# Optimization experiments

Measured on AMD Instinct MI355X. Metric: run time of the kernel, lower is better.

The kernel has to match this reference:

```python
import jax, jax.numpy as jnp
import numpy as np

N_WIRES = 13
N_LAYERS = 3
N_OUT = 10
T = 1.0
BATCH = 512
DIM = 2 ** N_WIRES
TWO_PI = 2.0 * np.pi

# Z eigenvalue table: Z_TAB[s, i] = +1 if bit of wire i in basis state s is 0 else -1.
# PennyLane convention: wire 0 is the most-significant bit of the statevector index.
_bits = (np.arange(DIM)[:, None] >> (N_WIRES - 1 - np.arange(N_WIRES))) & 1
Z_TAB = jnp.asarray(1.0 - 2.0 * _bits, dtype=jnp.float32)        # (DIM, n)
ZZ_TAB = Z_TAB * jnp.roll(Z_TAB, -1, axis=1)                     # z_i * z_{(i+1)%n}


def rot_matrix(phi, theta, omega):
    # qml.Rot = RZ(omega) @ RY(theta) @ RZ(phi)
    c = jnp.cos(theta / 2)
    s = jnp.sin(theta / 2)
    ep = jnp.exp(-0.5j * (phi + omega).astype(jnp.complex64))
    em = jnp.exp(-0.5j * (phi - omega).astype(jnp.complex64))
    row0 = jnp.stack([ep * c, -jnp.conj(em) * s])
    row1 = jnp.stack([em * s, jnp.conj(ep) * c])
    return jnp.stack([row0, row1])  # (2, 2) complex64


def apply_1q(state, U, w):
    # state: (B, 2, 2, ..., 2); apply 2x2 gate U on wire w (axis w+1)
    st = jnp.moveaxis(state, w + 1, 1)
    st = jnp.einsum('ab,xb...->xa...', U, st)
    return jnp.moveaxis(st, 1, w + 1)


def apply_cnot(state, c, t):
    # flip target axis where control bit == 1
    st = jnp.moveaxis(state, (c + 1, t + 1), (1, 2))
    st = jnp.concatenate([st[:, :1], st[:, 1:, ::-1]], axis=1)
    return jnp.moveaxis(st, (1, 2), (c + 1, t + 1))


def _forward(inputs, weights, embed_weights):
    B = inputs.shape[0]
    # Hadamard on every wire from |0...0> -> uniform superposition
    psi = jnp.full((B, DIM), DIM ** -0.5, dtype=jnp.complex64)
    for l in range(N_LAYERS):
        # --- Hamiltonian encoding: diagonal phase exp(-i t (sum (w x + b) Z_i + sum g Z_i Z_{i+1}))
        omega = embed_weights[l, :, 0]
        bias = embed_weights[l, :, 1]
        gamma = embed_weights[l, :, 2]
        coeff = inputs * omega + bias                              # (B, n)
        ang = T * (coeff @ Z_TAB.T + gamma @ ZZ_TAB.T)             # (B, DIM)
        psi = psi * jnp.exp((-1j) * ang.astype(jnp.complex64))
        # --- StronglyEntanglingLayers, single layer (range 1)
        st = psi.reshape((B,) + (2,) * N_WIRES)
        for i in range(N_WIRES):
            U = rot_matrix(weights[l, i, 0], weights[l, i, 1], weights[l, i, 2])
            st = apply_1q(st, U, i)
        for i in range(N_WIRES):
            st = apply_cnot(st, i, (i + 1) % N_WIRES)
        psi = st.reshape(B, DIM)
    probs = psi.real ** 2 + psi.imag ** 2                          # (B, DIM)
    return probs @ Z_TAB[:, :N_OUT]                                # <Z_i>, (B, N_OUT)


def setup_inputs() -> dict:
    key = jax.random.key(0)
    k1, k2, k3 = jax.random.split(key, 3)
    inputs = jax.random.normal(k1, (BATCH, N_WIRES), dtype=jnp.float32)
    weights = jax.random.uniform(k2, (N_LAYERS, N_WIRES, 3), dtype=jnp.float32) * TWO_PI
    embed_weights = jax.random.uniform(k3, (N_LAYERS, N_WIRES, 3), dtype=jnp.float32) * TWO_PI
    return {"inputs": inputs, "weights": weights, "embed_weights": embed_weights}


def reference(inputs, weights, embed_weights):
    return _forward(inputs, weights, embed_weights)
```

## Files before the change

kernel.cpp:

```cpp
#include <hip/hip_runtime.h>
#include <math.h>

#define N_WIRES 13
#define DIM 8192
#define N_LAYERS 3
#define N_OUT 10
#define BATCH 512
#define NTHREADS 512

typedef float v2f __attribute__((ext_vector_type(2)));

#define CMUL_PK(d, u, a) do { \
    asm("v_pk_mul_f32 %0, %1, %2 op_sel:[0,0] op_sel_hi:[0,1]" \
        : "=v"(d) : "v"(u), "v"(a)); \
    asm("v_pk_fma_f32 %0, %1, %2, %0 op_sel:[1,1,0] op_sel_hi:[1,0,1] neg_lo:[0,1,0]" \
        : "+v"(d) : "v"(u), "v"(a)); \
} while (0)

#define CFMA_PK(d, u, a) do { \
    asm("v_pk_fma_f32 %0, %1, %2, %0 op_sel:[0,0,0] op_sel_hi:[0,1,1]" \
        : "+v"(d) : "v"(u), "v"(a)); \
    asm("v_pk_fma_f32 %0, %1, %2, %0 op_sel:[1,1,0] op_sel_hi:[1,0,1] neg_lo:[0,1,0]" \
        : "+v"(d) : "v"(u), "v"(a)); \
} while (0)

__device__ __forceinline__ void bfly(v2f& a0, v2f& a1,
                                     v2f u00, v2f u01, v2f u10, v2f u11) {
    v2f n0, n1;
    CMUL_PK(n0, u00, a0); CFMA_PK(n0, u01, a1);
    CMUL_PK(n1, u10, a0); CFMA_PK(n1, u11, a1);
    a0 = n0; a1 = n1;
}

#define REG_GATE(MASK, W) do { \
    const float4 uA = uu4[l][W][0]; \
    const float4 uB = uu4[l][W][1]; \
    const v2f u00 = {uA.x, uA.y}, u01 = {uA.z, uA.w}; \
    const v2f u10 = {uB.x, uB.y}, u11 = {uB.z, uB.w}; \
    _Pragma("unroll") \
    for (int k0 = 0; k0 < 16; ++k0) { \
        if (k0 & (MASK)) continue; \
        bfly(a[k0], a[k0 | (MASK)], u00, u01, u10, u11); \
    } \
} while (0)

#define SWZ1_GATE(W) do { \
    const float4 uA = uu4[l][W][0]; \
    const float4 uB = uu4[l][W][1]; \
    const bool hb = (tid & 1) != 0; \
    const v2f ua = hb ? (v2f){uB.z, uB.w} : (v2f){uA.x, uA.y}; \
    const v2f up = hb ? (v2f){uB.x, uB.y} : (v2f){uA.z, uA.w}; \
    _Pragma("unroll") \
    for (int k = 0; k < 16; ++k) { \
        v2f p; \
        p.x = __int_as_float(__builtin_amdgcn_ds_swizzle(__float_as_int(a[k].x), 0x041F)); \
        p.y = __int_as_float(__builtin_amdgcn_ds_swizzle(__float_as_int(a[k].y), 0x041F)); \
        v2f n; CMUL_PK(n, ua, a[k]); CFMA_PK(n, up, p); \
        a[k] = n; \
    } \
} while (0)

__global__ __launch_bounds__(NTHREADS, 2) void vqc_kernel(
    const float* __restrict__ inputs,
    const float* __restrict__ weights,
    const float* __restrict__ embed,
    float* __restrict__ out)
{
    __shared__ v2f  s2[DIM];
    __shared__ float4 uu4[N_LAYERS][N_WIRES][2];
    __shared__ float  co[N_LAYERS][N_WIRES];
    __shared__ float  ga[N_LAYERS][N_WIRES];
    __shared__ v2f  Ek[N_LAYERS][16];
    __shared__ v2f  Eh[N_LAYERS][8];
    __shared__ v2f  El[N_LAYERS][64];
    __shared__ v2f  G3[N_LAYERS], G12[N_LAYERS], G6[N_LAYERS];
    __shared__ float red[NTHREADS / 64][N_OUT];

    const int b   = blockIdx.x;
    const int tid = threadIdx.x;

    if (tid < N_LAYERS * N_WIRES) {
        const int l = tid / N_WIRES;
        const int w = tid - l * N_WIRES;
        const int base = (l * N_WIRES + w) * 3;
        const float om = embed[base + 0];
        const float bi = embed[base + 1];
        const float gm = embed[base + 2];
        co[l][w] = inputs[b * N_WIRES + w] * om + bi;
        ga[l][w] = gm;

        const float phi = weights[base + 0];
        const float th  = weights[base + 1];
        const float omg = weights[base + 2];
        float c, s, ca, sa, cb, sb;
        __sincosf(0.5f * th, &s, &c);
        __sincosf(0.5f * (phi + omg), &sa, &ca);
        __sincosf(0.5f * (phi - omg), &sb, &cb);
        uu4[l][w][0] = make_float4( ca * c, -sa * c, -cb * s, -sb * s);
        uu4[l][w][1] = make_float4( cb * s, -sb * s,  ca * c,  sa * c);

        if (w == 3 || w == 6 || w == 12) {
            float s2v, c2v; __sincosf(2.f * gm, &s2v, &c2v);
            if (w == 3)  G3[l]  = (v2f){c2v, s2v};
            if (w == 6)  G6[l]  = (v2f){c2v, s2v};
            if (w == 12) G12[l] = (v2f){c2v, s2v};
        }
    }
    __syncthreads();

    if (tid < N_LAYERS * 16) {
        const int l = tid >> 4, k = tid & 15;
        float S = 0.f;
        #pragma unroll
        for (int w = 0; w < N_WIRES; ++w) S += co[l][w] + ga[l][w];
        const int b3 = (k >> 3) & 1, b2 = (k >> 2) & 1, b1 = (k >> 1) & 1, b0 = k & 1;
        float v = S;
        if (b3) v -= 2.f * co[l][0];
        if (b2) v -= 2.f * co[l][1];
        if (b1) v -= 2.f * co[l][2];
        if (b0) v -= 2.f * co[l][3];
        if (b3 ^ b2) v -= 2.f * ga[l][0];
        if (b2 ^ b1) v -= 2.f * ga[l][1];
        if (b1 ^ b0) v -= 2.f * ga[l][2];
        float sv, cv; __sincosf(v, &sv, &cv);
        const float sc = (l == 0) ? 0.011048543456039806f : 1.f;
        Ek[l][k] = (v2f){sc * cv, -sc * sv};
    }
    if (tid >= 64 && tid < 64 + N_LAYERS * 8) {
        const int t = tid - 64, l = t >> 3, h = t & 7;
        const int b8 = (h >> 2) & 1, b7 = (h >> 1) & 1, b6 = h & 1;
        float T = 0.f;
        if (b8) T += co[l][4];
        if (b7) T += co[l][5];
        if (b6) T += co[l][6];
        if (b8 ^ b7) T += ga[l][4];
        if (b7 ^ b6) T += ga[l][5];
        float sv, cv; __sincosf(2.f * T, &sv, &cv);
        Eh[l][h] = (v2f){cv, sv};
    }
    if (tid >= 128 && tid < 128 + N_LAYERS * 64) {
        const int t = tid - 128, l = t >> 6, m = t & 63;
        const int b5 = (m >> 5) & 1, b4 = (m >> 4) & 1, b3 = (m >> 3) & 1;
        const int b2 = (m >> 2) & 1, b1 = (m >> 1) & 1, b0 = m & 1;
        float T = 0.f;
        if (b5) T += co[l][7];
        if (b4) T += co[l][8];
        if (b3) T += co[l][9];
        if (b2) T += co[l][10];
        if (b1) T += co[l][11];
        if (b0) T += co[l][12];
        if (b5 ^ b4) T += ga[l][7];
        if (b4 ^ b3) T += ga[l][8];
        if (b3 ^ b2) T += ga[l][9];
        if (b2 ^ b1) T += ga[l][10];
        if (b1 ^ b0) T += ga[l][11];
        float sv, cv; __sincosf(2.f * T, &sv, &cv);
        El[l][m] = (v2f){cv, sv};
    }
    __syncthreads();

    const int tidA   = tid ^ ((tid >> 5) & 0xE);
    const int baseB  = ((tid >> 5) << 9) | (tid & 31);
    const int xbaseC = ((tid >> 1) << 5) | (tid & 1);
    const int baseC  = xbaseC ^ ((tid >> 1) & 0xE);
    const bool t8 = ((tid >> 8) & 1) != 0;
    const bool t0 = (tid & 1) != 0;
    const bool cG6 = (((tid >> 6) ^ (tid >> 5)) & 1) != 0;
    const int hidx = (tid >> 6) & 7;
    const int lidx = tid & 63;

    v2f a[16];

    #pragma unroll 1
    for (int l = 0; l < N_LAYERS; ++l) {
        v2f ep; CMUL_PK(ep, Eh[l][hidx], El[l][lidx]);
        { v2f t6; CMUL_PK(t6, ep, G6[l]); ep = cG6 ? t6 : ep; }
        v2f eg3; CMUL_PK(eg3, ep, G3[l]);
        const v2f P0 = t8 ? eg3 : ep,  P1 = t8 ? ep : eg3;
        const v2f one = {1.f, 0.f};
        const v2f Q0 = t0 ? G12[l] : one, Q1 = t0 ? one : G12[l];
        v2f R00, R01, R10, R11;
        CMUL_PK(R00, P0, Q0);
        CMUL_PK(R01, P0, Q1);
        CMUL_PK(R10, P1, Q0);
        CMUL_PK(R11, P1, Q1);

        if (l == 0) {
            #pragma unroll
            for (int k = 0; k < 16; ++k) {
                const v2f Rk = (k & 1) ? ((k & 8) ? R11 : R10) : ((k & 8) ? R01 : R00);
                CMUL_PK(a[k], Rk, Ek[l][k]);
            }
        } else {
            #pragma unroll
            for (int k = 0; k < 16; ++k) {
                const v2f Rk = (k & 1) ? ((k & 8) ? R11 : R10) : ((k & 8) ? R01 : R00);
                v2f f; CMUL_PK(f, Rk, Ek[l][k]);
                const v2f v = s2[tidA | (k << 9)];
                CMUL_PK(a[k], v, f);
            }
        }

        REG_GATE(8, 0);
        REG_GATE(4, 1);
        REG_GATE(2, 2);
        REG_GATE(1, 3);

        #pragma unroll
        for (int k = 0; k < 16; ++k)
            s2[tidA | (k << 9)] = a[k];
        __syncthreads();

        #pragma unroll
        for (int k = 0; k < 16; ++k)
            a[k] = s2[baseB ^ ((k << 5) | (k & 0xE))];
        REG_GATE(8, 4);
        REG_GATE(4, 5);
        REG_GATE(2, 6);
        REG_GATE(1, 7);
        #pragma unroll
        for (int k = 0; k < 16; ++k)
            s2[baseB ^ ((k << 5) | (k & 0xE))] = a[k];
        __syncthreads();

        #pragma unroll
        for (int k = 0; k < 16; ++k)
            a[k] = s2[baseC ^ (k << 1)];
        if (l < N_LAYERS - 1) __syncthreads();

        REG_GATE(8, 8);
        REG_GATE(4, 9);
        REG_GATE(2, 10);
        REG_GATE(1, 11);
        SWZ1_GATE(12);

        if (l < N_LAYERS - 1) {
            #pragma unroll
            for (int k = 0; k < 16; ++k) {
                const int x = xbaseC | (k << 1);
                int t = x ^ (x >> 1); t ^= t >> 2; t ^= t >> 4; t ^= t >> 8;
                const int y = (t & 0x0FFF) | (((t ^ (x >> 12)) & 1) << 12);
                s2[y ^ ((y >> 5) & 0xE)] = a[k];
            }
            __syncthreads();
        }
    }

    float acc[N_OUT];
    #pragma unroll
    for (int o = 0; o < N_OUT; ++o) acc[o] = 0.f;

    #pragma unroll
    for (int k = 0; k < 16; ++k) {
        const int x = xbaseC | (k << 1);
        int t = x ^ (x >> 1); t ^= t >> 2; t ^= t >> 4; t ^= t >> 8;
        const int y = (t & 0x0FFF) | (((t ^ (x >> 12)) & 1) << 12);
        const float p = a[k].x * a[k].x + a[k].y * a[k].y;
        #pragma unroll
        for (int o = 0; o < N_OUT; ++o)
            acc[o] += ((y >> (12 - o)) & 1) ? -p : p;
    }

    #pragma unroll
    for (int off = 32; off >= 1; off >>= 1) {
        #pragma unroll
        for (int o = 0; o < N_OUT; ++o) acc[o] += __shfl_down(acc[o], off);
    }
    const int wave = tid >> 6;
    const int lane = tid & 63;
    if (lane == 0) {
        #pragma unroll
        for (int o = 0; o < N_OUT; ++o) red[wave][o] = acc[o];
    }
    __syncthreads();
    if (tid < N_OUT) {
        float s = 0.f;
        #pragma unroll
        for (int w = 0; w < NTHREADS / 64; ++w) s += red[w][tid];
        out[b * N_OUT + tid] = s;
    }
}

extern "C" void kernel_launch(void* const* d_in, const int* in_sizes, int n_in,
                              void* d_out, int out_size, void* d_ws, size_t ws_size,
                              hipStream_t stream) {
    const float* inputs  = (const float*)d_in[0];
    const float* weights = (const float*)d_in[1];
    const float* embed   = (const float*)d_in[2];
    float* out = (float*)d_out;
    vqc_kernel<<<BATCH, NTHREADS, 0, stream>>>(inputs, weights, embed, out);
}
```

Measured before the change: 52.60 us.

## Double threads per block, hold 8 amplitudes per thread with four gate phases

The block grows from 512 to 1024 threads, so each thread keeps 8 amplitudes in registers instead of 16. The 12 register-resident wire gates are regrouped from three phases of four wires into four phases of three, each with new swizzled shared-memory index maps. The diagonal phase tables are resplit to match (Ek over 3 wires, Eh over 4). This halves register pressure per thread and adds parallelism, at the cost of one extra shared-memory round trip and barrier per layer, and of larger blocks that need wider synchronisation.

Result: faster. 47.49 us (-9.7%).

```diff
diff --git a/kernel.cpp b/kernel.cpp
--- a/kernel.cpp
+++ b/kernel.cpp
@@ -6,7 +6,9 @@
 #define N_LAYERS 3
 #define N_OUT 10
 #define BATCH 512
-#define NTHREADS 512
+#define NTHREADS 1024
+#define NAMPS 8
+#define NWAVES (NTHREADS / 64)
 
 typedef float v2f __attribute__((ext_vector_type(2)));
 
@@ -38,7 +40,7 @@
     const v2f u00 = {uA.x, uA.y}, u01 = {uA.z, uA.w}; \
     const v2f u10 = {uB.x, uB.y}, u11 = {uB.z, uB.w}; \
     _Pragma("unroll") \
-    for (int k0 = 0; k0 < 16; ++k0) { \
+    for (int k0 = 0; k0 < NAMPS; ++k0) { \
         if (k0 & (MASK)) continue; \
         bfly(a[k0], a[k0 | (MASK)], u00, u01, u10, u11); \
     } \
@@ -51,7 +53,7 @@
     const v2f ua = hb ? (v2f){uB.z, uB.w} : (v2f){uA.x, uA.y}; \
     const v2f up = hb ? (v2f){uB.x, uB.y} : (v2f){uA.z, uA.w}; \
     _Pragma("unroll") \
-    for (int k = 0; k < 16; ++k) { \
+    for (int k = 0; k < NAMPS; ++k) { \
         v2f p; \
         p.x = __int_as_float(__builtin_amdgcn_ds_swizzle(__float_as_int(a[k].x), 0x041F)); \
         p.y = __int_as_float(__builtin_amdgcn_ds_swizzle(__float_as_int(a[k].y), 0x041F)); \
@@ -60,7 +62,7 @@
     } \
 } while (0)
 
-__global__ __launch_bounds__(NTHREADS, 2) void vqc_kernel(
+__global__ __launch_bounds__(NTHREADS, 8) void vqc_kernel(
     const float* __restrict__ inputs,
     const float* __restrict__ weights,
     const float* __restrict__ embed,
@@ -70,11 +72,11 @@
     __shared__ float4 uu4[N_LAYERS][N_WIRES][2];
     __shared__ float  co[N_LAYERS][N_WIRES];
     __shared__ float  ga[N_LAYERS][N_WIRES];
-    __shared__ v2f  Ek[N_LAYERS][16];
-    __shared__ v2f  Eh[N_LAYERS][8];
+    __shared__ v2f  Ek[N_LAYERS][8];
+    __shared__ v2f  Eh[N_LAYERS][16];
     __shared__ v2f  El[N_LAYERS][64];
-    __shared__ v2f  G3[N_LAYERS], G12[N_LAYERS], G6[N_LAYERS];
-    __shared__ float red[NTHREADS / 64][N_OUT];
+    __shared__ v2f  G2[N_LAYERS], G6b[N_LAYERS], G12[N_LAYERS];
+    __shared__ float red[NWAVES][N_OUT];
 
     const int b   = blockIdx.x;
     const int tid = threadIdx.x;
@@ -99,42 +101,42 @@
         uu4[l][w][0] = make_float4( ca * c, -sa * c, -cb * s, -sb * s);
         uu4[l][w][1] = make_float4( cb * s, -sb * s,  ca * c,  sa * c);
 
-        if (w == 3 || w == 6 || w == 12) {
+        if (w == 2 || w == 6 || w == 12) {
             float s2v, c2v; __sincosf(2.f * gm, &s2v, &c2v);
-            if (w == 3)  G3[l]  = (v2f){c2v, s2v};
-            if (w == 6)  G6[l]  = (v2f){c2v, s2v};
+            if (w == 2)  G2[l]  = (v2f){c2v, s2v};
+            if (w == 6)  G6b[l] = (v2f){c2v, s2v};
             if (w == 12) G12[l] = (v2f){c2v, s2v};
         }
     }
     __syncthreads();
 
-    if (tid < N_LAYERS * 16) {
-        const int l = tid >> 4, k = tid & 15;
+    if (tid < N_LAYERS * 8) {
+        const int l = tid >> 3, k = tid & 7;
         float S = 0.f;
         #pragma unroll
         for (int w = 0; w < N_WIRES; ++w) S += co[l][w] + ga[l][w];
-        const int b3 = (k >> 3) & 1, b2 = (k >> 2) & 1, b1 = (k >> 1) & 1, b0 = k & 1;
+        const int b2 = (k >> 2) & 1, b1 = (k >> 1) & 1, b0 = k & 1;
         float v = S;
-        if (b3) v -= 2.f * co[l][0];
-        if (b2) v -= 2.f * co[l][1];
-        if (b1) v -= 2.f * co[l][2];
-        if (b0) v -= 2.f * co[l][3];
-        if (b3 ^ b2) v -= 2.f * ga[l][0];
-        if (b2 ^ b1) v -= 2.f * ga[l][1];
-        if (b1 ^ b0) v -= 2.f * ga[l][2];
+        if (b2) v -= 2.f * co[l][0];
+        if (b1) v -= 2.f * co[l][1];
+        if (b0) v -= 2.f * co[l][2];
+        if (b2 ^ b1) v -= 2.f * ga[l][0];
+        if (b1 ^ b0) v -= 2.f * ga[l][1];
         float sv, cv; __sincosf(v, &sv, &cv);
         const float sc = (l == 0) ? 0.011048543456039806f : 1.f;
         Ek[l][k] = (v2f){sc * cv, -sc * sv};
     }
-    if (tid >= 64 && tid < 64 + N_LAYERS * 8) {
-        const int t = tid - 64, l = t >> 3, h = t & 7;
-        const int b8 = (h >> 2) & 1, b7 = (h >> 1) & 1, b6 = h & 1;
+    if (tid >= 64 && tid < 64 + N_LAYERS * 16) {
+        const int t = tid - 64, l = t >> 4, h = t & 15;
+        const int h3 = (h >> 3) & 1, h2 = (h >> 2) & 1, h1 = (h >> 1) & 1, h0 = h & 1;
         float T = 0.f;
-        if (b8) T += co[l][4];
-        if (b7) T += co[l][5];
-        if (b6) T += co[l][6];
-        if (b8 ^ b7) T += ga[l][4];
-        if (b7 ^ b6) T += ga[l][5];
+        if (h3) T += co[l][3];
+        if (h2) T += co[l][4];
+        if (h1) T += co[l][5];
+        if (h0) T += co[l][6];
+        if (h3 ^ h2) T += ga[l][3];
+        if (h2 ^ h1) T += ga[l][4];
+        if (h1 ^ h0) T += ga[l][5];
         float sv, cv; __sincosf(2.f * T, &sv, &cv);
         Eh[l][h] = (v2f){cv, sv};
     }
@@ -159,24 +161,28 @@
     }
     __syncthreads();
 
-    const int tidA   = tid ^ ((tid >> 5) & 0xE);
-    const int baseB  = ((tid >> 5) << 9) | (tid & 31);
-    const int xbaseC = ((tid >> 1) << 5) | (tid & 1);
-    const int baseC  = xbaseC ^ ((tid >> 1) & 0xE);
-    const bool t8 = ((tid >> 8) & 1) != 0;
+    const int tA = tid ^ (((tid >> 5) & 7) << 1);
+    const int bB = (((tid >> 7) << 10) | (tid & 127))
+                 ^ ((((tid >> 6) & 1) << 2) | (((tid >> 5) & 1) << 1));
+    const int bC = (((tid >> 4) << 7) | (tid & 15))
+                 ^ (((tid >> 4) & 1) << 3);
+    const int bD = (((tid >> 1) << 4) | (tid & 1))
+                 ^ (((tid >> 2) & 7) << 1);
+    const int xD = ((tid >> 1) << 4) | (tid & 1);
+    const bool t9 = ((tid >> 9) & 1) != 0;
     const bool t0 = (tid & 1) != 0;
-    const bool cG6 = (((tid >> 6) ^ (tid >> 5)) & 1) != 0;
-    const int hidx = (tid >> 6) & 7;
+    const bool c6 = (((tid >> 6) ^ (tid >> 5)) & 1) != 0;
+    const int hidx = (tid >> 6) & 15;
     const int lidx = tid & 63;
 
-    v2f a[16];
+    v2f a[NAMPS];
 
     #pragma unroll 1
     for (int l = 0; l < N_LAYERS; ++l) {
         v2f ep; CMUL_PK(ep, Eh[l][hidx], El[l][lidx]);
-        { v2f t6; CMUL_PK(t6, ep, G6[l]); ep = cG6 ? t6 : ep; }
-        v2f eg3; CMUL_PK(eg3, ep, G3[l]);
-        const v2f P0 = t8 ? eg3 : ep,  P1 = t8 ? ep : eg3;
+        { v2f tb; CMUL_PK(tb, ep, G6b[l]); ep = c6 ? tb : ep; }
+        v2f eg2; CMUL_PK(eg2, ep, G2[l]);
+        const v2f P0 = t9 ? eg2 : ep,  P1 = t9 ? ep : eg2;
         const v2f one = {1.f, 0.f};
         const v2f Q0 = t0 ? G12[l] : one, Q1 = t0 ? one : G12[l];
         v2f R00, R01, R10, R11;
@@ -187,48 +193,55 @@
 
         if (l == 0) {
             #pragma unroll
-            for (int k = 0; k < 16; ++k) {
-                const v2f Rk = (k & 1) ? ((k & 8) ? R11 : R10) : ((k & 8) ? R01 : R00);
+            for (int k = 0; k < NAMPS; ++k) {
+                const v2f Rk = (k & 1) ? ((k & 4) ? R11 : R10) : ((k & 4) ? R01 : R00);
                 CMUL_PK(a[k], Rk, Ek[l][k]);
             }
         } else {
             #pragma unroll
-            for (int k = 0; k < 16; ++k) {
-                const v2f Rk = (k & 1) ? ((k & 8) ? R11 : R10) : ((k & 8) ? R01 : R00);
+            for (int k = 0; k < NAMPS; ++k) {
+                const v2f Rk = (k & 1) ? ((k & 4) ? R11 : R10) : ((k & 4) ? R01 : R00);
                 v2f f; CMUL_PK(f, Rk, Ek[l][k]);
-                const v2f v = s2[tidA | (k << 9)];
+                const v2f v = s2[(k << 10) | tA];
                 CMUL_PK(a[k], v, f);
             }
         }
 
-        REG_GATE(8, 0);
-        REG_GATE(4, 1);
-        REG_GATE(2, 2);
-        REG_GATE(1, 3);
-
-        #pragma unroll
-        for (int k = 0; k < 16; ++k)
-            s2[tidA | (k << 9)] = a[k];
+        REG_GATE(4, 0);
+        REG_GATE(2, 1);
+        REG_GATE(1, 2);
+        #pragma unroll
+        for (int k = 0; k < NAMPS; ++k)
+            s2[(k << 10) | tA] = a[k];
         __syncthreads();
 
         #pragma unroll
-        for (int k = 0; k < 16; ++k)
-            a[k] = s2[baseB ^ ((k << 5) | (k & 0xE))];
-        REG_GATE(8, 4);
-        REG_GATE(4, 5);
-        REG_GATE(2, 6);
-        REG_GATE(1, 7);
-        #pragma unroll
-        for (int k = 0; k < 16; ++k)
-            s2[baseB ^ ((k << 5) | (k & 0xE))] = a[k];
+        for (int k = 0; k < NAMPS; ++k)
+            a[k] = s2[bB ^ (k << 7) ^ ((k & 1) << 3)];
+        REG_GATE(4, 3);
+        REG_GATE(2, 4);
+        REG_GATE(1, 5);
+        #pragma unroll
+        for (int k = 0; k < NAMPS; ++k)
+            s2[bB ^ (k << 7) ^ ((k & 1) << 3)] = a[k];
         __syncthreads();
 
         #pragma unroll
-        for (int k = 0; k < 16; ++k)
-            a[k] = s2[baseC ^ (k << 1)];
+        for (int k = 0; k < NAMPS; ++k)
+            a[k] = s2[bC ^ (k << 4) ^ (k & 6)];
+        REG_GATE(4, 6);
+        REG_GATE(2, 7);
+        REG_GATE(1, 8);
+        #pragma unroll
+        for (int k = 0; k < NAMPS; ++k)
+            s2[bC ^ (k << 4) ^ (k & 6)] = a[k];
+        __syncthreads();
+
+        #pragma unroll
+        for (int k = 0; k < NAMPS; ++k)
+            a[k] = s2[bD ^ (k << 1)];
         if (l < N_LAYERS - 1) __syncthreads();
 
-        REG_GATE(8, 8);
         REG_GATE(4, 9);
         REG_GATE(2, 10);
         REG_GATE(1, 11);
@@ -236,11 +249,11 @@
 
         if (l < N_LAYERS - 1) {
             #pragma unroll
-            for (int k = 0; k < 16; ++k) {
-                const int x = xbaseC | (k << 1);
+            for (int k = 0; k < NAMPS; ++k) {
+                const int x = xD | (k << 1);
                 int t = x ^ (x >> 1); t ^= t >> 2; t ^= t >> 4; t ^= t >> 8;
                 const int y = (t & 0x0FFF) | (((t ^ (x >> 12)) & 1) << 12);
-                s2[y ^ ((y >> 5) & 0xE)] = a[k];
+                s2[y ^ (((y >> 5) & 7) << 1)] = a[k];
             }
             __syncthreads();
         }
@@ -251,8 +264,8 @@
     for (int o = 0; o < N_OUT; ++o) acc[o] = 0.f;
 
     #pragma unroll
-    for (int k = 0; k < 16; ++k) {
-        const int x = xbaseC | (k << 1);
+    for (int k = 0; k < NAMPS; ++k) {
+        const int x = xD | (k << 1);
         int t = x ^ (x >> 1); t ^= t >> 2; t ^= t >> 4; t ^= t >> 8;
         const int y = (t & 0x0FFF) | (((t ^ (x >> 12)) & 1) << 12);
         const float p = a[k].x * a[k].x + a[k].y * a[k].y;
@@ -276,7 +289,7 @@
     if (tid < N_OUT) {
         float s = 0.f;
         #pragma unroll
-        for (int w = 0; w < NTHREADS / 64; ++w) s += red[w][tid];
+        for (int w = 0; w < NWAVES; ++w) s += red[w][tid];
         out[b * N_OUT + tid] = s;
     }
 }
```
